# Kernel optimization log

Measured on AMD Instinct MI355X. Metric: run time of the kernel, lower is better.

Reference implementation:

```python
import jax, jax.numpy as jnp
import numpy as np

B, N, K, C, COND = 8, 2048, 32, 256, 512
LN_EPS = 1e-5


def setup_inputs() -> dict:
    key = jax.random.key(0)
    ks = jax.random.split(key, 8)
    node_feats = jax.random.normal(ks[0], (B, N, C), jnp.float32)
    cond_feats = jax.random.normal(ks[1], (B, COND), jnp.float32)
    W_cond = jax.random.normal(ks[2], (COND, 2 * C), jnp.float32) * 0.02
    b_cond = jnp.zeros((2 * C,), jnp.float32)
    W_film = jax.random.normal(ks[3], (C, C), jnp.float32) * 0.05
    b_film = jnp.zeros((C,), jnp.float32)
    weights = jax.random.uniform(ks[4], (B, N * K, 1), jnp.float32)
    params = jax.random.uniform(ks[5], (B, N * K, 1), jnp.float32)
    coords = jax.random.randint(ks[6], (B * N * K,), 0, B * N, jnp.int64)
    return dict(node_feats=node_feats, cond_feats=cond_feats, W_cond=W_cond,
                b_cond=b_cond, W_film=W_film, b_film=b_film,
                weights=weights, params=params, coords=coords)


def reference(node_feats, cond_feats, W_cond, b_cond, W_film, b_film,
              weights, params, coords):
    # FiLM conditioning: gamma/beta from cond projection  [B, 2C] -> two [B, C]
    gb = cond_feats @ W_cond + b_cond
    gamma, beta = jnp.split(gb, 2, axis=-1)
    gamma = gamma + 1.0
    # film_l: linear -> layernorm (no affine) -> FiLM -> relu
    h = node_feats @ W_film + b_film                      # [B, N, C]
    mu = jnp.mean(h, axis=-1, keepdims=True)
    var = jnp.mean(jnp.square(h - mu), axis=-1, keepdims=True)
    h = (h - mu) * jax.lax.rsqrt(var + LN_EPS)
    new_node_feats = jax.nn.relu(h * gamma[:, None, :] + beta[:, None, :])
    # edge weights: elementwise product, reshape to [B, N, K, 1]
    ew = (weights * params).reshape(B, N, K, 1)
    # gather neighbor feats by flat coords over B*N, then weighted segment-sum over K
    node_j = new_node_feats.reshape(B * N, C)[coords].reshape(B, N, K, C)
    nb_feats = jnp.sum(ew * node_j, axis=2)               # [B, N, C]
    # non-loop op, no GIN: residual add then relu (norm_l is identity)
    return jax.nn.relu(new_node_feats + nb_feats)
```

## Files before the change

### kernel.cpp

```cpp
#include <hip/hip_runtime.h>


typedef unsigned short u16;
typedef unsigned int u32;

typedef __attribute__((ext_vector_type(8))) __bf16 bf16x8;
typedef __attribute__((ext_vector_type(4))) float f32x4;
typedef __attribute__((ext_vector_type(2))) float f32x2;

__device__ __forceinline__ float b2f(u16 u) {
  union { u32 i; float f; } x; x.i = ((u32)u) << 16; return x.f;
}
__device__ __forceinline__ u16 f2b(float f) {
  union { float f; u32 i; } x; x.f = f;
  u32 r = (x.i + 0x7fffu + ((x.i >> 16) & 1u)) >> 16;
  return (u16)r;
}

__global__ __launch_bounds__(256) void k_prep(const float* __restrict__ Wf,
                                              u16* __restrict__ Wp,
                                              const float* __restrict__ cond,
                                              const float* __restrict__ Wc,
                                              float* __restrict__ gbp,
                                              const float* __restrict__ wts,
                                              const float* __restrict__ prm,
                                              float* __restrict__ ew) {
  int blk = blockIdx.x;
  int tid = threadIdx.x;
  if (blk < 32) {
    int i0 = blk * 2048 + tid;
    #pragma unroll
    for (int u = 0; u < 8; ++u) {
      int i = i0 + u * 256;
      int j  = i & 7;
      int l  = (i >> 3) & 63;
      int ks = (i >> 9) & 7;
      int ct = i >> 12;
      int k   = ks * 32 + ((l >> 4) << 3) + j;
      int col = ct * 16 + (l & 15);
      Wp[i] = f2b(Wf[k * 256 + col]);
    }
  } else if (blk < 64) {
    int idx = blk - 32;
    int b  = idx >> 2;
    int kh = (idx >> 1) & 1;
    int ch = idx & 1;
    int j  = ch * 256 + tid;
    __shared__ float cf[256];
    cf[tid] = cond[b * 512 + kh * 256 + tid];
    __syncthreads();
    float a = 0.f;
    #pragma unroll 8
    for (int i = 0; i < 256; ++i)
      a += cf[i] * Wc[(kh * 256 + i) * 512 + j];
    gbp[(kh * 8 + b) * 512 + j] = a;
  } else {
    int i0 = (blk - 64) * 16384 + tid * 4;
    #pragma unroll
    for (int u = 0; u < 16; ++u) {
      int e = i0 + u * 1024;
      f32x4 w = *(const f32x4*)(wts + e);
      f32x4 p = *(const f32x4*)(prm + e);
      f32x4 r = w * p;
      *(f32x4*)(ew + e) = r;
    }
  }
}

__global__ __launch_bounds__(256) void k_film(const float* __restrict__ A,
                                              const u16* __restrict__ Wp,
                                              const float* __restrict__ bfm,
                                              const float* __restrict__ gbp,
                                              const float* __restrict__ bcond,
                                              u16* __restrict__ nnf) {
  const int tid = threadIdx.x;
  const int l = tid & 63;
  const int w = tid >> 6;
  const int row0 = blockIdx.x * 32;
  const int b = row0 >> 11;

  __shared__ u16 As[32 * 264];
  __shared__ float red[4][2][4][2][4];

  #pragma unroll
  for (int u = 0; u < 8; ++u) {
    int f = u * 256 + tid;
    int row = f >> 6;
    int col = (f & 63) * 4;
    f32x4 v = *(const f32x4*)(A + (size_t)(row0 + row) * 256 + col);
    u16* dst = As + row * 264 + col;
    dst[0] = f2b(v.x); dst[1] = f2b(v.y); dst[2] = f2b(v.z); dst[3] = f2b(v.w);
  }
  __syncthreads();

  f32x4 acc[2][4];
  #pragma unroll
  for (int rb = 0; rb < 2; ++rb)
    #pragma unroll
    for (int c = 0; c < 4; ++c) {
      acc[rb][c].x = 0.f; acc[rb][c].y = 0.f;
      acc[rb][c].z = 0.f; acc[rb][c].w = 0.f;
    }

  const u16* asrc = As + (l & 15) * 264 + ((l >> 4) << 3);
  const u16* wl = Wp + (size_t)l * 8;

  #pragma unroll
  for (int ks = 0; ks < 8; ++ks) {
    bf16x8 af0 = *(const bf16x8*)(asrc + ks * 32);
    bf16x8 af1 = *(const bf16x8*)(asrc + 16 * 264 + ks * 32);
    #pragma unroll
    for (int c = 0; c < 4; ++c) {
      int ct = w * 4 + c;
      bf16x8 bfr = *(const bf16x8*)(wl + ((size_t)(ct * 8 + ks)) * 512);
      acc[0][c] = __builtin_amdgcn_mfma_f32_16x16x32_bf16(af0, bfr, acc[0][c], 0, 0, 0);
      acc[1][c] = __builtin_amdgcn_mfma_f32_16x16x32_bf16(af1, bfr, acc[1][c], 0, 0, 0);
    }
  }

  const int g = l >> 4;
  #pragma unroll
  for (int rb = 0; rb < 2; ++rb) {
    float s[4] = {0.f, 0.f, 0.f, 0.f};
    float q[4] = {0.f, 0.f, 0.f, 0.f};
    #pragma unroll
    for (int c = 0; c < 4; ++c) {
      float bcol = bfm[(w * 4 + c) * 16 + (l & 15)];
      #pragma unroll
      for (int r = 0; r < 4; ++r) {
        float v = acc[rb][c][r] + bcol;
        acc[rb][c][r] = v;
        s[r] += v;
        q[r] += v * v;
      }
    }
    #pragma unroll
    for (int m = 1; m < 16; m <<= 1) {
      #pragma unroll
      for (int r = 0; r < 4; ++r) {
        s[r] += __shfl_xor(s[r], m);
        q[r] += __shfl_xor(q[r], m);
      }
    }
    if ((l & 15) == 0) {
      #pragma unroll
      for (int r = 0; r < 4; ++r) {
        red[w][rb][g][0][r] = s[r];
        red[w][rb][g][1][r] = q[r];
      }
    }
  }
  __syncthreads();

  #pragma unroll
  for (int rb = 0; rb < 2; ++rb) {
    float mu[4], rs[4];
    #pragma unroll
    for (int r = 0; r < 4; ++r) {
      float ss = red[0][rb][g][0][r] + red[1][rb][g][0][r] +
                 red[2][rb][g][0][r] + red[3][rb][g][0][r];
      float qq = red[0][rb][g][1][r] + red[1][rb][g][1][r] +
                 red[2][rb][g][1][r] + red[3][rb][g][1][r];
      mu[r] = ss * (1.0f / 256.0f);
      float var = qq * (1.0f / 256.0f) - mu[r] * mu[r];
      rs[r] = rsqrtf(var + 1e-5f);
    }
    const int rowb = row0 + rb * 16 + (g << 2);
    #pragma unroll
    for (int c = 0; c < 4; ++c) {
      int col = (w * 4 + c) * 16 + (l & 15);
      float ga = gbp[b * 512 + col] + gbp[(8 + b) * 512 + col] + bcond[col] + 1.0f;
      float be = gbp[b * 512 + 256 + col] + gbp[(8 + b) * 512 + 256 + col] + bcond[256 + col];
      #pragma unroll
      for (int r = 0; r < 4; ++r) {
        float h = (acc[rb][c][r] - mu[r]) * rs[r];
        nnf[(size_t)(rowb + r) * 256 + col] = f2b(fmaxf(h * ga + be, 0.f));
      }
    }
  }
}

__global__ __launch_bounds__(256) void k_gather(const u16* __restrict__ nnf,
                                                const float* __restrict__ ew,
                                                const int* __restrict__ coords,
                                                float* __restrict__ out) {
  int q  = blockIdx.x >> 11;
  int bi = blockIdx.x & 2047;
  int wv = threadIdx.x >> 6;
  int lane = threadIdx.x & 63;
  int h = lane >> 5;
  int m = lane & 31;
  int row = bi * 8 + wv * 2 + h;

  int e = row * 32 + m;
  int idx_l  = __builtin_nontemporal_load(coords + e);
  float ew_l = __builtin_nontemporal_load(ew + e);

  const u16* colp = nnf + q * 64 + m * 2;

  u32 v[32];
  #pragma unroll
  for (int k = 0; k < 32; ++k) {
    int idx = __shfl(idx_l, k, 32);
    v[k] = *(const u32*)(colp + ((size_t)idx << 8));
  }

  float a0 = 0.f, a1 = 0.f;
  #pragma unroll
  for (int k = 0; k < 32; ++k) {
    float w = __shfl(ew_l, k, 32);
    a0 += w * b2f((u16)(v[k] & 0xffff));
    a1 += w * b2f((u16)(v[k] >> 16));
  }

  u32 sv = *(const u32*)(colp + ((size_t)row << 8));
  f32x2 o;
  o.x = fmaxf(b2f((u16)(sv & 0xffff)) + a0, 0.f);
  o.y = fmaxf(b2f((u16)(sv >> 16)) + a1, 0.f);
  __builtin_nontemporal_store(o, (f32x2*)(out + (size_t)row * 256 + q * 64 + m * 2));
}

extern "C" void kernel_launch(void* const* d_in, const int* in_sizes, int n_in,
                              void* d_out, int out_size, void* d_ws, size_t ws_size,
                              hipStream_t stream) {
  const float* node = (const float*)d_in[0];
  const float* cond = (const float*)d_in[1];
  const float* Wc   = (const float*)d_in[2];
  const float* bc   = (const float*)d_in[3];
  const float* Wf   = (const float*)d_in[4];
  const float* bf   = (const float*)d_in[5];
  const float* wts  = (const float*)d_in[6];
  const float* prm  = (const float*)d_in[7];
  const int* coords = (const int*)d_in[8];
  float* out = (float*)d_out;

  char* ws = (char*)d_ws;
  float* gbp = (float*)ws;
  u16* Wp    = (u16*)(ws + 32768);
  float* ew  = (float*)(ws + 32768 + 131072);
  u16* nnf   = (u16*)(ws + 32768 + 131072 + 2097152);

  k_prep<<<dim3(96), dim3(256), 0, stream>>>(Wf, Wp, cond, Wc, gbp, wts, prm, ew);
  k_film<<<dim3(512), dim3(256), 0, stream>>>(node, Wp, bf, gbp, bc, nnf);
  k_gather<<<dim3(8192), dim3(256), 0, stream>>>(nnf, ew, coords, out);
}
```

Baseline: 55.58 us.

## Fuse edge-weight product into gather and use one row per wave

Drops the separate edge-weight multiply pass in the prep kernel and computes weights*params inside the gather kernel, removing a 2 MB workspace write and re-read. The gather is restructured so each wave handles one row with 64 lanes covering 64 columns as single bf16 loads, broadcasting indices and weights via readlane instead of 32-wide shuffles. This doubles the block count and makes each gathered access 128 bytes per wave instead of 256 split across two half-waves. The cost is more, smaller memory transactions and more redundant index/weight loads per column.

```diff
diff --git a/kernel.cpp b/kernel.cpp
--- a/kernel.cpp
+++ b/kernel.cpp
@@ -6,7 +6,6 @@
 
 typedef __attribute__((ext_vector_type(8))) __bf16 bf16x8;
 typedef __attribute__((ext_vector_type(4))) float f32x4;
-typedef __attribute__((ext_vector_type(2))) float f32x2;
 
 __device__ __forceinline__ float b2f(u16 u) {
   union { u32 i; float f; } x; x.i = ((u32)u) << 16; return x.f;
@@ -21,10 +20,7 @@
                                               u16* __restrict__ Wp,
                                               const float* __restrict__ cond,
                                               const float* __restrict__ Wc,
-                                              float* __restrict__ gbp,
-                                              const float* __restrict__ wts,
-                                              const float* __restrict__ prm,
-                                              float* __restrict__ ew) {
+                                              float* __restrict__ gbp) {
   int blk = blockIdx.x;
   int tid = threadIdx.x;
   if (blk < 32) {
@@ -40,7 +36,7 @@
       int col = ct * 16 + (l & 15);
       Wp[i] = f2b(Wf[k * 256 + col]);
     }
-  } else if (blk < 64) {
+  } else {
     int idx = blk - 32;
     int b  = idx >> 2;
     int kh = (idx >> 1) & 1;
@@ -54,16 +50,6 @@
     for (int i = 0; i < 256; ++i)
       a += cf[i] * Wc[(kh * 256 + i) * 512 + j];
     gbp[(kh * 8 + b) * 512 + j] = a;
-  } else {
-    int i0 = (blk - 64) * 16384 + tid * 4;
-    #pragma unroll
-    for (int u = 0; u < 16; ++u) {
-      int e = i0 + u * 1024;
-      f32x4 w = *(const f32x4*)(wts + e);
-      f32x4 p = *(const f32x4*)(prm + e);
-      f32x4 r = w * p;
-      *(f32x4*)(ew + e) = r;
-    }
   }
 }
 
@@ -181,43 +167,40 @@
 }
 
 __global__ __launch_bounds__(256) void k_gather(const u16* __restrict__ nnf,
-                                                const float* __restrict__ ew,
+                                                const float* __restrict__ wts,
+                                                const float* __restrict__ prm,
                                                 const int* __restrict__ coords,
                                                 float* __restrict__ out) {
-  int q  = blockIdx.x >> 11;
-  int bi = blockIdx.x & 2047;
+  int q  = blockIdx.x >> 12;
+  int bi = blockIdx.x & 4095;
   int wv = threadIdx.x >> 6;
   int lane = threadIdx.x & 63;
-  int h = lane >> 5;
-  int m = lane & 31;
-  int row = bi * 8 + wv * 2 + h;
-
-  int e = row * 32 + m;
+  int row = bi * 4 + wv;
+
+  int e = row * 32 + (lane & 31);
   int idx_l  = __builtin_nontemporal_load(coords + e);
-  float ew_l = __builtin_nontemporal_load(ew + e);
-
-  const u16* colp = nnf + q * 64 + m * 2;
+  float ew_l = __builtin_nontemporal_load(wts + e) *
+               __builtin_nontemporal_load(prm + e);
+
+  const u16* colp = nnf + q * 64 + lane;
 
   u32 v[32];
   #pragma unroll
   for (int k = 0; k < 32; ++k) {
-    int idx = __shfl(idx_l, k, 32);
-    v[k] = *(const u32*)(colp + ((size_t)idx << 8));
-  }
-
-  float a0 = 0.f, a1 = 0.f;
+    int sidx = __builtin_amdgcn_readlane(idx_l, k);
+    v[k] = colp[(size_t)sidx << 8];
+  }
+
+  float acc = 0.f;
   #pragma unroll
   for (int k = 0; k < 32; ++k) {
-    float w = __shfl(ew_l, k, 32);
-    a0 += w * b2f((u16)(v[k] & 0xffff));
-    a1 += w * b2f((u16)(v[k] >> 16));
-  }
-
-  u32 sv = *(const u32*)(colp + ((size_t)row << 8));
-  f32x2 o;
-  o.x = fmaxf(b2f((u16)(sv & 0xffff)) + a0, 0.f);
-  o.y = fmaxf(b2f((u16)(sv >> 16)) + a1, 0.f);
-  __builtin_nontemporal_store(o, (f32x2*)(out + (size_t)row * 256 + q * 64 + m * 2));
+    float w = __int_as_float(__builtin_amdgcn_readlane(__float_as_int(ew_l), k));
+    acc += w * b2f((u16)v[k]);
+  }
+
+  float self = b2f((u16)colp[(size_t)row << 8]);
+  float o = fmaxf(self + acc, 0.f);
+  __builtin_nontemporal_store(o, out + (size_t)row * 256 + q * 64 + lane);
 }
 
 extern "C" void kernel_launch(void* const* d_in, const int* in_sizes, int n_in,
@@ -237,10 +220,9 @@
   char* ws = (char*)d_ws;
   float* gbp = (float*)ws;
   u16* Wp    = (u16*)(ws + 32768);
-  float* ew  = (float*)(ws + 32768 + 131072);
-  u16* nnf   = (u16*)(ws + 32768 + 131072 + 2097152);
-
-  k_prep<<<dim3(96), dim3(256), 0, stream>>>(Wf, Wp, cond, Wc, gbp, wts, prm, ew);
+  u16* nnf   = (u16*)(ws + 32768 + 131072);
+
+  k_prep<<<dim3(64), dim3(256), 0, stream>>>(Wf, Wp, cond, Wc, gbp);
   k_film<<<dim3(512), dim3(256), 0, stream>>>(node, Wp, bf, gbp, bc, nnf);
-  k_gather<<<dim3(8192), dim3(256), 0, stream>>>(nnf, ew, coords, out);
-}
+  k_gather<<<dim3(16384), dim3(256), 0, stream>>>(nnf, wts, prm, coords, out);
+}
```

Result: slower. 58.89 us (+6.0%).
